# Performance work log

Measured on AMD Instinct MI355X. Metric: run time of the kernel, lower is better.

## Reference

```python
import jax, jax.numpy as jnp
import numpy as np

N = 100000   # total nodes
E = 1600000  # total edges
G = 1000     # graphs in batch
NPG = N // G # nodes per graph
IN = 128
HID = 128
LBL = 100
EMB = 32


def setup_inputs() -> dict:
    key = jax.random.key(0)
    ks = jax.random.split(key, 12)
    x = jax.random.normal(ks[0], (N, IN), dtype=jnp.float32)
    edge_index = jax.random.randint(ks[1], (2, E), 0, N, dtype=jnp.int32)
    drnl = jax.random.randint(ks[2], (N,), 0, LBL, dtype=jnp.int32)
    batch = (jnp.arange(N, dtype=jnp.int32) // NPG)
    target_local = jax.random.randint(ks[3], (2 * G,), 0, NPG, dtype=jnp.int32)
    ptr = jnp.arange(G + 1, dtype=jnp.int32) * NPG
    s = 0.02
    emb = s * jax.random.normal(ks[4], (LBL, EMB), dtype=jnp.float32)
    W1 = s * jax.random.normal(ks[5], (IN + EMB, HID), dtype=jnp.float32)
    b1 = jnp.zeros((HID,), jnp.float32)
    W2 = s * jax.random.normal(ks[6], (HID, HID), dtype=jnp.float32)
    b2 = jnp.zeros((HID,), jnp.float32)
    Wm1 = s * jax.random.normal(ks[7], (HID * 5, HID), dtype=jnp.float32)
    bm1 = jnp.zeros((HID,), jnp.float32)
    Wm2 = s * jax.random.normal(ks[8], (HID, 2), dtype=jnp.float32)
    bm2 = jnp.zeros((2,), jnp.float32)
    return {"x": x, "emb": emb, "W1": W1, "b1": b1, "W2": W2, "b2": b2,
            "Wm1": Wm1, "bm1": bm1, "Wm2": Wm2, "bm2": bm2,
            "edge_index": edge_index, "drnl": drnl, "batch": batch,
            "target_local": target_local, "ptr": ptr}


def gcn_conv(h, W, b, src, dst, n):
    # PyG GCNConv: linear, add self-loops, symmetric deg norm, scatter-add, bias
    hw = h @ W
    deg = jax.ops.segment_sum(jnp.ones(src.shape[0], hw.dtype), dst,
                              num_segments=n) + 1.0  # +1 for self loop
    dinv = jax.lax.rsqrt(deg)
    norm = dinv[src] * dinv[dst]          # [E]
    msg = hw[src] * norm[:, None]          # [E, hid] gather + scale
    agg = jax.ops.segment_sum(msg, dst, num_segments=n)
    agg = agg + hw * (dinv * dinv)[:, None]  # self-loop message
    return agg + b


def reference(x, emb, W1, b1, W2, b2, Wm1, bm1, Wm2, bm2,
              edge_index, drnl, batch, target_local, ptr):
    src, dst = edge_index[0], edge_index[1]
    n = x.shape[0]
    z = jnp.concatenate([x, emb[drnl]], axis=1)          # [N, in+32]
    z = jax.nn.relu(gcn_conv(z, W1, b1, src, dst, n))    # [N, hid]
    z = jax.nn.relu(gcn_conv(z, W2, b2, src, dst, n))    # [N, hid]
    g = ptr.shape[0] - 1
    h_pool = jax.ops.segment_max(z, batch, num_segments=g)  # global_max_pool
    uv = target_local.reshape(g, 2) + ptr[:-1, None]     # global node ids
    h_u = z[uv[:, 0]]
    h_v = z[uv[:, 1]]
    feats = jnp.concatenate([h_u, h_v, jnp.abs(h_u - h_v), h_u * h_v, h_pool],
                            axis=1)                      # [G, 5*hid]
    hidm = jax.nn.relu(feats @ Wm1 + bm1)
    logits = hidm @ Wm2 + bm2                            # [G, 2]
    return logits
```

## Files before the change

### kernel.cpp

```cpp
#include <hip/hip_runtime.h>
#include <hip/hip_bf16.h>
#include <math.h>

static inline size_t align_up(size_t x, size_t a) { return (x + a - 1) / a * a; }

typedef short bf16x8 __attribute__((ext_vector_type(8)));
typedef float f32x4 __attribute__((ext_vector_type(4)));
typedef unsigned short u16x8 __attribute__((ext_vector_type(8)));
typedef int i32x4 __attribute__((ext_vector_type(4)));


#define NBUCK 512
#define BCAP 8192

__global__ __launch_bounds__(256) void bin_kernel(
    const int* __restrict__ src, const int* __restrict__ dst,
    int* __restrict__ bcnt, long long* __restrict__ staging, int E) {
  __shared__ int lcnt[NBUCK];
  __shared__ int gbase[NBUCK];
  __shared__ int lidx[NBUCK];
  const int tid = threadIdx.x;
  const int base = blockIdx.x * 4096;
  lcnt[tid] = 0; lcnt[tid + 256] = 0;
  lidx[tid] = 0; lidx[tid + 256] = 0;
  __syncthreads();
#pragma unroll
  for (int j = 0; j < 4; ++j) {
    const int idx = base + j * 1024 + tid * 4;
    if (idx + 3 < E) {
      const i32x4 d4 = __builtin_nontemporal_load((const i32x4*)(dst + idx));
#pragma unroll
      for (int c = 0; c < 4; ++c) atomicAdd(&lcnt[d4[c] >> 8], 1);
    } else {
      for (int c = 0; c < 4; ++c)
        if (idx + c < E) atomicAdd(&lcnt[dst[idx + c] >> 8], 1);
    }
  }
  __syncthreads();
  {
    const int c0 = lcnt[tid];
    if (c0 > 0) gbase[tid] = atomicAdd(&bcnt[tid], c0);
    const int c1 = lcnt[tid + 256];
    if (c1 > 0) gbase[tid + 256] = atomicAdd(&bcnt[tid + 256], c1);
  }
  __syncthreads();
#pragma unroll
  for (int j = 0; j < 4; ++j) {
    const int idx = base + j * 1024 + tid * 4;
    if (idx + 3 < E) {
      const i32x4 d4 = __builtin_nontemporal_load((const i32x4*)(dst + idx));
      const i32x4 s4 = __builtin_nontemporal_load((const i32x4*)(src + idx));
#pragma unroll
      for (int c = 0; c < 4; ++c) {
        const int d = d4[c];
        const int bkt = d >> 8;
        const int i = atomicAdd(&lidx[bkt], 1);
        const int pos = gbase[bkt] + i;
        if (pos < BCAP)
          staging[(size_t)bkt * BCAP + pos] =
              (long long)(((unsigned long long)(unsigned)s4[c] << 32) | (unsigned)d);
      }
    } else {
      for (int c = 0; c < 4; ++c) {
        if (idx + c < E) {
          const int d = dst[idx + c];
          const int bkt = d >> 8;
          const int i = atomicAdd(&lidx[bkt], 1);
          const int pos = gbase[bkt] + i;
          if (pos < BCAP)
            staging[(size_t)bkt * BCAP + pos] =
                (long long)(((unsigned long long)(unsigned)src[idx + c] << 32) | (unsigned)d);
        }
      }
    }
  }
}

__global__ __launch_bounds__(512) void bscan_kernel(const int* __restrict__ bcnt,
                                                    int* __restrict__ bbase,
                                                    int* __restrict__ rowptr, int N, int E) {
  __shared__ int sm[NBUCK];
  const int t = threadIdx.x;
  const int v = bcnt[t];
  sm[t] = v;
  __syncthreads();
  for (int o = 1; o < NBUCK; o <<= 1) {
    int x = (t >= o) ? sm[t - o] : 0;
    __syncthreads();
    sm[t] += x;
    __syncthreads();
  }
  bbase[t] = sm[t] - v;
  if (t == 0) rowptr[N] = E;
}

__global__ __launch_bounds__(256) void csr_kernel(
    const long long* __restrict__ staging, const int* __restrict__ bcnt,
    const int* __restrict__ bbase, int* __restrict__ rowptr,
    float* __restrict__ dinv, int* __restrict__ esrc, int N) {
  __shared__ int c1[256];
  __shared__ int off[256];
  __shared__ int sm[256];
  const int b = blockIdx.x;
  const int tid = threadIdx.x;
  const int cnt = min(bcnt[b], BCAP);
  const int base = bbase[b];
  const long long* sp = staging + (size_t)b * BCAP;
  c1[tid] = 0;
  __syncthreads();
  for (int i = tid; i < cnt; i += 256) {
    const int d8 = ((int)sp[i]) & 255;
    atomicAdd(&c1[d8], 1);
  }
  __syncthreads();
  const int deg = c1[tid];
  sm[tid] = deg;
  __syncthreads();
  for (int o = 1; o < 256; o <<= 1) {
    int x = (tid >= o) ? sm[tid - o] : 0;
    __syncthreads();
    sm[tid] += x;
    __syncthreads();
  }
  off[tid] = sm[tid] - deg;
  const int node = b * 256 + tid;
  if (node < N) {
    rowptr[node] = base + off[tid];
    dinv[node] = rsqrtf((float)(deg + 1));
  }
  c1[tid] = 0;
  __syncthreads();
  for (int i = tid; i < cnt; i += 256) {
    const long long pr = sp[i];
    const int d8 = ((int)pr) & 255;
    const int idx = atomicAdd(&c1[d8], 1);
    esrc[base + off[d8] + idx] = (int)(unsigned)((unsigned long long)pr >> 32);
  }
}


__device__ __forceinline__ void bf16_split(float x, unsigned short& hi, unsigned short& lo) {
  unsigned u = __float_as_uint(x);
  unsigned r = (u + 0x7fffu + ((u >> 16) & 1u)) & 0xffff0000u;
  hi = (unsigned short)(r >> 16);
  float rem = x - __uint_as_float(r);
  unsigned u2 = __float_as_uint(rem);
  unsigned r2 = u2 + 0x7fffu + ((u2 >> 16) & 1u);
  lo = (unsigned short)(r2 >> 16);
}

__device__ __forceinline__ unsigned short bf16_rtn(float x) {
  unsigned u = __float_as_uint(x);
  return (unsigned short)((u + 0x7fffu + ((u >> 16) & 1u)) >> 16);
}

__global__ void wsplit_kernel(const float* __restrict__ W1, const float* __restrict__ W2,
                              unsigned short* __restrict__ w1hi, unsigned short* __restrict__ w1lo,
                              unsigned short* __restrict__ w2hi, unsigned short* __restrict__ w2lo) {
  int i = blockIdx.x * blockDim.x + threadIdx.x;
  const int t1 = 160 * 128;
  const int t2 = 128 * 128;
  const float* W;
  unsigned short *whi, *wlo;
  if (i < t1) {
    W = W1; whi = w1hi; wlo = w1lo;
  } else {
    i -= t1;
    if (i >= t2) return;
    W = W2; whi = w2hi; wlo = w2lo;
  }
  int k = i >> 7;
  int n = i & 127;
  unsigned short h, l;
  bf16_split(W[i], h, l);
  size_t idx = ((size_t)(((k >> 5) * 128 + n) * 4 + ((k >> 3) & 3)) << 3) + (k & 7);
  whi[idx] = h;
  wlo[idx] = l;
}


__global__ __launch_bounds__(512) void gemm_mfma_kernel(
    const float* __restrict__ A, const float* __restrict__ emb,
    const int* __restrict__ drnl,
    const unsigned short* __restrict__ whi, const unsigned short* __restrict__ wlo,
    unsigned short* __restrict__ outb, int n, int K) {
  __shared__ unsigned short smem[16896];
  const int tid = threadIdx.x;
  const int row0 = blockIdx.x * 128;
  const int w = tid >> 6;
  const int l = tid & 63;
  const int r = l & 15;
  const int q = l >> 4;
  const int grow = row0 + (w << 4) + r;
  const bool rowok = grow < n;
  const int nks = K >> 5;

  int embrow = 0;
  if (K > 128 && rowok) embrow = drnl[grow];

  f32x4 acc[8];
#pragma unroll
  for (int ct = 0; ct < 8; ++ct) {
    acc[ct][0] = 0.f; acc[ct][1] = 0.f; acc[ct][2] = 0.f; acc[ct][3] = 0.f;
  }

  u16x8 bst_h = *(const u16x8*)(whi + (size_t)tid * 8);
  u16x8 bst_l = *(const u16x8*)(wlo + (size_t)tid * 8);

  for (int ks = 0; ks < nks; ++ks) {
    const int k0 = (ks << 5) + (q << 3);
    float4 a0 = make_float4(0.f, 0.f, 0.f, 0.f), a1 = a0;
    if (rowok) {
      if (k0 < 128) {
        const float* ap = A + (size_t)grow * 128 + k0;
        a0 = *(const float4*)ap;
        a1 = *(const float4*)(ap + 4);
      } else {
        const float* ep = emb + (size_t)embrow * 32 + (k0 - 128);
        a0 = *(const float4*)ep;
        a1 = *(const float4*)(ep + 4);
      }
    }
    bf16x8 ah, al;
    {
      unsigned short h, lo_;
      bf16_split(a0.x, h, lo_); ah[0] = (short)h; al[0] = (short)lo_;
      bf16_split(a0.y, h, lo_); ah[1] = (short)h; al[1] = (short)lo_;
      bf16_split(a0.z, h, lo_); ah[2] = (short)h; al[2] = (short)lo_;
      bf16_split(a0.w, h, lo_); ah[3] = (short)h; al[3] = (short)lo_;
      bf16_split(a1.x, h, lo_); ah[4] = (short)h; al[4] = (short)lo_;
      bf16_split(a1.y, h, lo_); ah[5] = (short)h; al[5] = (short)lo_;
      bf16_split(a1.z, h, lo_); ah[6] = (short)h; al[6] = (short)lo_;
      bf16_split(a1.w, h, lo_); ah[7] = (short)h; al[7] = (short)lo_;
    }

    if (ks) __syncthreads();
    *(u16x8*)&smem[tid * 8] = bst_h;
    *(u16x8*)&smem[4096 + tid * 8] = bst_l;
    __syncthreads();

    if (ks + 1 < nks) {
      bst_h = *(const u16x8*)(whi + (size_t)(ks + 1) * 4096 + (size_t)tid * 8);
      bst_l = *(const u16x8*)(wlo + (size_t)(ks + 1) * 4096 + (size_t)tid * 8);
    }

#pragma unroll
    for (int ct = 0; ct < 8; ++ct) {
      const int boff = ((ct << 4) + r) * 32 + (q << 3);
      const bf16x8 bh = *(const bf16x8*)&smem[boff];
      const bf16x8 bl = *(const bf16x8*)&smem[4096 + boff];
      acc[ct] = __builtin_amdgcn_mfma_f32_16x16x32_bf16(ah, bh, acc[ct], 0, 0, 0);
      acc[ct] = __builtin_amdgcn_mfma_f32_16x16x32_bf16(al, bh, acc[ct], 0, 0, 0);
      acc[ct] = __builtin_amdgcn_mfma_f32_16x16x32_bf16(ah, bl, acc[ct], 0, 0, 0);
    }
  }

  __syncthreads();
#pragma unroll
  for (int ct = 0; ct < 8; ++ct) {
    const int col = (ct << 4) + r;
#pragma unroll
    for (int j = 0; j < 4; ++j) {
      const int row = (w << 4) + (q << 2) + j;
      smem[row * 132 + col] = bf16_rtn(acc[ct][j]);
    }
  }
  __syncthreads();
#pragma unroll
  for (int p = 0; p < 4; ++p) {
    const int idx = p * 512 + tid;
    const int row = idx >> 4;
    const int c8 = (idx & 15) * 8;
    const int gr = row0 + row;
    if (gr < n) {
      u16x8 v = *(const u16x8*)&smem[row * 132 + c8];
      *(u16x8*)(outb + (size_t)gr * 128 + c8) = v;
    }
  }
}


__global__ __launch_bounds__(512) void gemm_bf16a_kernel(
    const unsigned short* __restrict__ Ab,
    const unsigned short* __restrict__ whi, const unsigned short* __restrict__ wlo,
    unsigned short* __restrict__ outb, int n) {
  __shared__ unsigned short smem[16896];
  const int tid = threadIdx.x;
  const int row0 = blockIdx.x * 128;
  const int w = tid >> 6;
  const int l = tid & 63;
  const int r = l & 15;
  const int q = l >> 4;
  const int grow = row0 + (w << 4) + r;
  const bool rowok = grow < n;
  const int nks = 4;

  f32x4 acc[8];
#pragma unroll
  for (int ct = 0; ct < 8; ++ct) {
    acc[ct][0] = 0.f; acc[ct][1] = 0.f; acc[ct][2] = 0.f; acc[ct][3] = 0.f;
  }

  u16x8 bst_h = *(const u16x8*)(whi + (size_t)tid * 8);
  u16x8 bst_l = *(const u16x8*)(wlo + (size_t)tid * 8);

  for (int ks = 0; ks < nks; ++ks) {
    const int k0 = (ks << 5) + (q << 3);
    bf16x8 ah = {0,0,0,0,0,0,0,0};
    if (rowok) ah = *(const bf16x8*)(Ab + (size_t)grow * 128 + k0);

    if (ks) __syncthreads();
    *(u16x8*)&smem[tid * 8] = bst_h;
    *(u16x8*)&smem[4096 + tid * 8] = bst_l;
    __syncthreads();

    if (ks + 1 < nks) {
      bst_h = *(const u16x8*)(whi + (size_t)(ks + 1) * 4096 + (size_t)tid * 8);
      bst_l = *(const u16x8*)(wlo + (size_t)(ks + 1) * 4096 + (size_t)tid * 8);
    }

#pragma unroll
    for (int ct = 0; ct < 8; ++ct) {
      const int boff = ((ct << 4) + r) * 32 + (q << 3);
      const bf16x8 bh = *(const bf16x8*)&smem[boff];
      const bf16x8 bl = *(const bf16x8*)&smem[4096 + boff];
      acc[ct] = __builtin_amdgcn_mfma_f32_16x16x32_bf16(ah, bh, acc[ct], 0, 0, 0);
      acc[ct] = __builtin_amdgcn_mfma_f32_16x16x32_bf16(ah, bl, acc[ct], 0, 0, 0);
    }
  }

  __syncthreads();
#pragma unroll
  for (int ct = 0; ct < 8; ++ct) {
    const int col = (ct << 4) + r;
#pragma unroll
    for (int j = 0; j < 4; ++j) {
      const int row = (w << 4) + (q << 2) + j;
      smem[row * 132 + col] = bf16_rtn(acc[ct][j]);
    }
  }
  __syncthreads();
#pragma unroll
  for (int p = 0; p < 4; ++p) {
    const int idx = p * 512 + tid;
    const int row = idx >> 4;
    const int c8 = (idx & 15) * 8;
    const int gr = row0 + row;
    if (gr < n) {
      u16x8 v = *(const u16x8*)&smem[row * 132 + c8];
      *(u16x8*)(outb + (size_t)gr * 128 + c8) = v;
    }
  }
}


__global__ __launch_bounds__(256) void agg_kernel(
    const unsigned* __restrict__ hwb, const int* __restrict__ rowptr,
    const int* __restrict__ esrc, const float* __restrict__ dinv,
    const float* __restrict__ bias, float* __restrict__ zf,
    unsigned* __restrict__ zb, int n, int obf16) {
  const int widx = (blockIdx.x * blockDim.x + threadIdx.x) >> 6;
  if (widx >= n) return;
  const int wid = __builtin_amdgcn_readfirstlane(widx);
  const int lane = threadIdx.x & 63;
  const int start = rowptr[wid];
  const int end = rowptr[wid + 1];
  const float dn = dinv[wid];
  float ax = 0.f, ay = 0.f;
  int e = start;
  for (; e + 4 <= end; e += 4) {
    const int s0 = esrc[e + 0];
    const int s1 = esrc[e + 1];
    const int s2 = esrc[e + 2];
    const int s3 = esrc[e + 3];
    const float d0 = dinv[s0];
    const float d1 = dinv[s1];
    const float d2 = dinv[s2];
    const float d3 = dinv[s3];
    const unsigned u0 = hwb[(size_t)s0 * 64 + lane];
    const unsigned u1 = hwb[(size_t)s1 * 64 + lane];
    const unsigned u2 = hwb[(size_t)s2 * 64 + lane];
    const unsigned u3 = hwb[(size_t)s3 * 64 + lane];
    const float w0 = d0 * dn;
    const float w1 = d1 * dn;
    const float w2 = d2 * dn;
    const float w3 = d3 * dn;
    ax = fmaf(__uint_as_float(u0 << 16), w0, ax);
    ay = fmaf(__uint_as_float(u0 & 0xffff0000u), w0, ay);
    ax = fmaf(__uint_as_float(u1 << 16), w1, ax);
    ay = fmaf(__uint_as_float(u1 & 0xffff0000u), w1, ay);
    ax = fmaf(__uint_as_float(u2 << 16), w2, ax);
    ay = fmaf(__uint_as_float(u2 & 0xffff0000u), w2, ay);
    ax = fmaf(__uint_as_float(u3 << 16), w3, ax);
    ay = fmaf(__uint_as_float(u3 & 0xffff0000u), w3, ay);
  }
  for (; e < end; ++e) {
    const int s0 = esrc[e];
    const float w0 = dinv[s0] * dn;
    const unsigned u0 = hwb[(size_t)s0 * 64 + lane];
    ax = fmaf(__uint_as_float(u0 << 16), w0, ax);
    ay = fmaf(__uint_as_float(u0 & 0xffff0000u), w0, ay);
  }
  const float sw = dn * dn;
  const unsigned us = hwb[(size_t)wid * 64 + lane];
  ax = fmaf(__uint_as_float(us << 16), sw, ax);
  ay = fmaf(__uint_as_float(us & 0xffff0000u), sw, ay);
  const float2 bb = ((const float2*)bias)[lane];
  float ox = ax + bb.x, oy = ay + bb.y;
  ox = ox > 0.f ? ox : 0.f;
  oy = oy > 0.f ? oy : 0.f;
  if (obf16) {
    const unsigned pw = ((unsigned)bf16_rtn(oy) << 16) | (unsigned)bf16_rtn(ox);
    zb[(size_t)wid * 64 + lane] = pw;
  } else {
    float2 o; o.x = ox; o.y = oy;
    ((float2*)zf)[(size_t)wid * 64 + lane] = o;
  }
}


__global__ __launch_bounds__(128) void final_kernel(
    const float* __restrict__ z, const int* __restrict__ tloc,
    const int* __restrict__ ptr,
    const float* __restrict__ Wm1, const float* __restrict__ bm1,
    const float* __restrict__ Wm2, const float* __restrict__ bm2,
    float* __restrict__ out, int npg) {
  __shared__ float feats[640];
  __shared__ float hid[128];
  const int g = blockIdx.x;
  const int t = threadIdx.x;
  const float* zbk = z + (size_t)g * npg * 128;
  float m = -INFINITY;
  for (int r = 0; r < npg; ++r) m = fmaxf(m, zbk[(size_t)r * 128 + t]);
  feats[512 + t] = m;
  const int base = ptr[g];
  const int u = base + tloc[2 * g];
  const int v = base + tloc[2 * g + 1];
  const float hu = z[(size_t)u * 128 + t];
  const float hv = z[(size_t)v * 128 + t];
  feats[t] = hu;
  feats[128 + t] = hv;
  feats[256 + t] = fabsf(hu - hv);
  feats[384 + t] = hu * hv;
  __syncthreads();
  float acc = bm1[t];
#pragma unroll 8
  for (int k = 0; k < 640; ++k) acc = fmaf(feats[k], Wm1[(size_t)k * 128 + t], acc);
  hid[t] = acc > 0.f ? acc : 0.f;
  __syncthreads();
  if (t < 2) {
    float a = bm2[t];
    for (int j = 0; j < 128; ++j) a = fmaf(hid[j], Wm2[j * 2 + t], a);
    out[g * 2 + t] = a;
  }
}


extern "C" void kernel_launch(void* const* d_in, const int* in_sizes, int n_in,
                              void* d_out, int out_size, void* d_ws, size_t ws_size,
                              hipStream_t stream) {
  const float* x   = (const float*)d_in[0];
  const float* emb = (const float*)d_in[1];
  const float* W1  = (const float*)d_in[2];
  const float* b1  = (const float*)d_in[3];
  const float* W2  = (const float*)d_in[4];
  const float* b2  = (const float*)d_in[5];
  const float* Wm1 = (const float*)d_in[6];
  const float* bm1 = (const float*)d_in[7];
  const float* Wm2 = (const float*)d_in[8];
  const float* bm2 = (const float*)d_in[9];
  const int* eidx  = (const int*)d_in[10];
  const int* drnl  = (const int*)d_in[11];
  const int* tloc  = (const int*)d_in[13];
  const int* ptr   = (const int*)d_in[14];
  float* out = (float*)d_out;

  const int N = in_sizes[11];
  const int E = in_sizes[10] / 2;
  const int G = in_sizes[13] / 2;
  const int NPG = N / G;
  const int* srcp = eidx;
  const int* dstp = eidx + E;

  char* w = (char*)d_ws;
  size_t o = 0;
  auto alloc = [&](size_t bytes) {
    void* p = w + o;
    o = align_up(o + bytes, 256);
    return p;
  };
  int*   rowptr = (int*)alloc((size_t)(N + 1) * 4);
  float* dinv   = (float*)alloc((size_t)N * 4);
  int*   bcnt   = (int*)alloc(NBUCK * 4);
  int*   bbase  = (int*)alloc(NBUCK * 4);
  int*   esrc   = (int*)alloc((size_t)E * 4);
  unsigned short* hwb = (unsigned short*)alloc((size_t)N * 128 * 2);
  unsigned short* zb16 = (unsigned short*)alloc((size_t)N * 128 * 2);
  float* z      = (float*)alloc((size_t)N * 128 * 4);
  long long* staging = (long long*)z;
  unsigned short* w1hi = (unsigned short*)alloc((size_t)160 * 128 * 2);
  unsigned short* w1lo = (unsigned short*)alloc((size_t)160 * 128 * 2);
  unsigned short* w2hi = (unsigned short*)alloc((size_t)128 * 128 * 2);
  unsigned short* w2lo = (unsigned short*)alloc((size_t)128 * 128 * 2);

  const int nch = (E + 4095) / 4096;
  const int nbk = (N + 255) / 256;

  hipMemsetAsync(bcnt, 0, NBUCK * 4, stream);
  bin_kernel<<<nch, 256, 0, stream>>>(srcp, dstp, bcnt, staging, E);
  bscan_kernel<<<1, NBUCK, 0, stream>>>(bcnt, bbase, rowptr, N, E);
  csr_kernel<<<nbk, 256, 0, stream>>>(staging, bcnt, bbase, rowptr, dinv, esrc, N);

  wsplit_kernel<<<(160 * 128 + 128 * 128 + 255) / 256, 256, 0, stream>>>(
      W1, W2, w1hi, w1lo, w2hi, w2lo);

  gemm_mfma_kernel<<<(N + 127) / 128, 512, 0, stream>>>(x, emb, drnl, w1hi, w1lo, hwb, N, 160);
  agg_kernel<<<(N * 64 + 255) / 256, 256, 0, stream>>>((const unsigned*)hwb, rowptr, esrc,
                                                       dinv, b1, nullptr, (unsigned*)zb16, N, 1);
  gemm_bf16a_kernel<<<(N + 127) / 128, 512, 0, stream>>>(zb16, w2hi, w2lo, hwb, N);
  agg_kernel<<<(N * 64 + 255) / 256, 256, 0, stream>>>((const unsigned*)hwb, rowptr, esrc,
                                                       dinv, b2, z, nullptr, N, 0);
  final_kernel<<<G, 128, 0, stream>>>(z, tloc, ptr, Wm1, bm1, Wm2, bm2, out, NPG);
}
```

Measured before the change: 277.3 us.

## Pack staging to 32 bits, fuse bucket scan, store final z as bf16, unroll aggregation

Edge staging entries shrink from 64-bit pairs to 32-bit words (src<<8 | low dst byte), halving staging traffic in binning and CSR build. The separate bucket scan kernel is removed: each CSR block now redundantly scans the 512 bucket counts itself, saving one launch. The second aggregation writes bf16 instead of fp32, so the pooling/readout kernel reads half the bytes, at some precision cost. The aggregation loop is unrolled to 8 edges with all gathers issued first to raise memory-level parallelism. The packing assumes source ids fit in 24 bits.

Result: faster. 270.2 us (-2.6%).

```diff
diff --git a/kernel.cpp b/kernel.cpp
--- a/kernel.cpp
+++ b/kernel.cpp
@@ -15,7 +15,7 @@
 
 __global__ __launch_bounds__(256) void bin_kernel(
     const int* __restrict__ src, const int* __restrict__ dst,
-    int* __restrict__ bcnt, long long* __restrict__ staging, int E) {
+    int* __restrict__ bcnt, unsigned* __restrict__ staging, int E) {
   __shared__ int lcnt[NBUCK];
   __shared__ int gbase[NBUCK];
   __shared__ int lidx[NBUCK];
@@ -58,7 +58,7 @@
         const int pos = gbase[bkt] + i;
         if (pos < BCAP)
           staging[(size_t)bkt * BCAP + pos] =
-              (long long)(((unsigned long long)(unsigned)s4[c] << 32) | (unsigned)d);
+              ((unsigned)s4[c] << 8) | ((unsigned)d & 255u);
       }
     } else {
       for (int c = 0; c < 4; ++c) {
@@ -69,55 +69,50 @@
           const int pos = gbase[bkt] + i;
           if (pos < BCAP)
             staging[(size_t)bkt * BCAP + pos] =
-                (long long)(((unsigned long long)(unsigned)src[idx + c] << 32) | (unsigned)d);
+                ((unsigned)src[idx + c] << 8) | ((unsigned)d & 255u);
         }
       }
     }
   }
 }
 
-__global__ __launch_bounds__(512) void bscan_kernel(const int* __restrict__ bcnt,
-                                                    int* __restrict__ bbase,
-                                                    int* __restrict__ rowptr, int N, int E) {
-  __shared__ int sm[NBUCK];
-  const int t = threadIdx.x;
-  const int v = bcnt[t];
-  sm[t] = v;
-  __syncthreads();
-  for (int o = 1; o < NBUCK; o <<= 1) {
-    int x = (t >= o) ? sm[t - o] : 0;
-    __syncthreads();
-    sm[t] += x;
-    __syncthreads();
-  }
-  bbase[t] = sm[t] - v;
-  if (t == 0) rowptr[N] = E;
-}
 
 __global__ __launch_bounds__(256) void csr_kernel(
-    const long long* __restrict__ staging, const int* __restrict__ bcnt,
-    const int* __restrict__ bbase, int* __restrict__ rowptr,
-    float* __restrict__ dinv, int* __restrict__ esrc, int N) {
+    const unsigned* __restrict__ staging, const int* __restrict__ bcnt,
+    int* __restrict__ rowptr, float* __restrict__ dinv, int* __restrict__ esrc,
+    int N, int E) {
+  __shared__ int sb[NBUCK];
   __shared__ int c1[256];
   __shared__ int off[256];
   __shared__ int sm[256];
   const int b = blockIdx.x;
   const int tid = threadIdx.x;
+  sb[tid] = bcnt[tid];
+  sb[tid + 256] = bcnt[tid + 256];
+  __syncthreads();
+  for (int o = 1; o < NBUCK; o <<= 1) {
+    const int x0 = (tid >= o) ? sb[tid - o] : 0;
+    const int x1 = (tid + 256 >= o) ? sb[tid + 256 - o] : 0;
+    __syncthreads();
+    sb[tid] += x0;
+    sb[tid + 256] += x1;
+    __syncthreads();
+  }
   const int cnt = min(bcnt[b], BCAP);
-  const int base = bbase[b];
-  const long long* sp = staging + (size_t)b * BCAP;
+  const int base = sb[b] - bcnt[b];
+  if (b == 0 && tid == 0) rowptr[N] = E;
+  const unsigned* sp = staging + (size_t)b * BCAP;
   c1[tid] = 0;
   __syncthreads();
   for (int i = tid; i < cnt; i += 256) {
-    const int d8 = ((int)sp[i]) & 255;
-    atomicAdd(&c1[d8], 1);
+    atomicAdd(&c1[sp[i] & 255u], 1);
   }
   __syncthreads();
   const int deg = c1[tid];
   sm[tid] = deg;
   __syncthreads();
   for (int o = 1; o < 256; o <<= 1) {
-    int x = (tid >= o) ? sm[tid - o] : 0;
+    const int x = (tid >= o) ? sm[tid - o] : 0;
     __syncthreads();
     sm[tid] += x;
     __syncthreads();
@@ -131,10 +126,10 @@
   c1[tid] = 0;
   __syncthreads();
   for (int i = tid; i < cnt; i += 256) {
-    const long long pr = sp[i];
-    const int d8 = ((int)pr) & 255;
+    const unsigned pr = sp[i];
+    const int d8 = (int)(pr & 255u);
     const int idx = atomicAdd(&c1[d8], 1);
-    esrc[base + off[d8] + idx] = (int)(unsigned)((unsigned long long)pr >> 32);
+    esrc[base + off[d8] + idx] = (int)(pr >> 8);
   }
 }
 
@@ -152,6 +147,10 @@
 __device__ __forceinline__ unsigned short bf16_rtn(float x) {
   unsigned u = __float_as_uint(x);
   return (unsigned short)((u + 0x7fffu + ((u >> 16) & 1u)) >> 16);
+}
+
+__device__ __forceinline__ float bf16_to_f(unsigned short v) {
+  return __uint_as_float((unsigned)v << 16);
 }
 
 __global__ void wsplit_kernel(const float* __restrict__ W1, const float* __restrict__ W2,
@@ -357,8 +356,7 @@
 __global__ __launch_bounds__(256) void agg_kernel(
     const unsigned* __restrict__ hwb, const int* __restrict__ rowptr,
     const int* __restrict__ esrc, const float* __restrict__ dinv,
-    const float* __restrict__ bias, float* __restrict__ zf,
-    unsigned* __restrict__ zb, int n, int obf16) {
+    const float* __restrict__ bias, unsigned* __restrict__ zb, int n) {
   const int widx = (blockIdx.x * blockDim.x + threadIdx.x) >> 6;
   if (widx >= n) return;
   const int wid = __builtin_amdgcn_readfirstlane(widx);
@@ -368,31 +366,22 @@
   const float dn = dinv[wid];
   float ax = 0.f, ay = 0.f;
   int e = start;
-  for (; e + 4 <= end; e += 4) {
-    const int s0 = esrc[e + 0];
-    const int s1 = esrc[e + 1];
-    const int s2 = esrc[e + 2];
-    const int s3 = esrc[e + 3];
-    const float d0 = dinv[s0];
-    const float d1 = dinv[s1];
-    const float d2 = dinv[s2];
-    const float d3 = dinv[s3];
-    const unsigned u0 = hwb[(size_t)s0 * 64 + lane];
-    const unsigned u1 = hwb[(size_t)s1 * 64 + lane];
-    const unsigned u2 = hwb[(size_t)s2 * 64 + lane];
-    const unsigned u3 = hwb[(size_t)s3 * 64 + lane];
-    const float w0 = d0 * dn;
-    const float w1 = d1 * dn;
-    const float w2 = d2 * dn;
-    const float w3 = d3 * dn;
-    ax = fmaf(__uint_as_float(u0 << 16), w0, ax);
-    ay = fmaf(__uint_as_float(u0 & 0xffff0000u), w0, ay);
-    ax = fmaf(__uint_as_float(u1 << 16), w1, ax);
-    ay = fmaf(__uint_as_float(u1 & 0xffff0000u), w1, ay);
-    ax = fmaf(__uint_as_float(u2 << 16), w2, ax);
-    ay = fmaf(__uint_as_float(u2 & 0xffff0000u), w2, ay);
-    ax = fmaf(__uint_as_float(u3 << 16), w3, ax);
-    ay = fmaf(__uint_as_float(u3 & 0xffff0000u), w3, ay);
+  for (; e + 8 <= end; e += 8) {
+    int s[8];
+#pragma unroll
+    for (int k = 0; k < 8; ++k) s[k] = esrc[e + k];
+    unsigned u[8];
+#pragma unroll
+    for (int k = 0; k < 8; ++k) u[k] = hwb[(size_t)s[k] * 64 + lane];
+    float dv[8];
+#pragma unroll
+    for (int k = 0; k < 8; ++k) dv[k] = dinv[s[k]];
+#pragma unroll
+    for (int k = 0; k < 8; ++k) {
+      const float wk = dv[k] * dn;
+      ax = fmaf(__uint_as_float(u[k] << 16), wk, ax);
+      ay = fmaf(__uint_as_float(u[k] & 0xffff0000u), wk, ay);
+    }
   }
   for (; e < end; ++e) {
     const int s0 = esrc[e];
@@ -409,18 +398,13 @@
   float ox = ax + bb.x, oy = ay + bb.y;
   ox = ox > 0.f ? ox : 0.f;
   oy = oy > 0.f ? oy : 0.f;
-  if (obf16) {
-    const unsigned pw = ((unsigned)bf16_rtn(oy) << 16) | (unsigned)bf16_rtn(ox);
-    zb[(size_t)wid * 64 + lane] = pw;
-  } else {
-    float2 o; o.x = ox; o.y = oy;
-    ((float2*)zf)[(size_t)wid * 64 + lane] = o;
-  }
+  const unsigned pw = ((unsigned)bf16_rtn(oy) << 16) | (unsigned)bf16_rtn(ox);
+  zb[(size_t)wid * 64 + lane] = pw;
 }
 
 
 __global__ __launch_bounds__(128) void final_kernel(
-    const float* __restrict__ z, const int* __restrict__ tloc,
+    const unsigned short* __restrict__ zb, const int* __restrict__ tloc,
     const int* __restrict__ ptr,
     const float* __restrict__ Wm1, const float* __restrict__ bm1,
     const float* __restrict__ Wm2, const float* __restrict__ bm2,
@@ -429,15 +413,15 @@
   __shared__ float hid[128];
   const int g = blockIdx.x;
   const int t = threadIdx.x;
-  const float* zbk = z + (size_t)g * npg * 128;
+  const unsigned short* zbk = zb + (size_t)g * npg * 128;
   float m = -INFINITY;
-  for (int r = 0; r < npg; ++r) m = fmaxf(m, zbk[(size_t)r * 128 + t]);
+  for (int r = 0; r < npg; ++r) m = fmaxf(m, bf16_to_f(zbk[(size_t)r * 128 + t]));
   feats[512 + t] = m;
   const int base = ptr[g];
   const int u = base + tloc[2 * g];
   const int v = base + tloc[2 * g + 1];
-  const float hu = z[(size_t)u * 128 + t];
-  const float hv = z[(size_t)v * 128 + t];
+  const float hu = bf16_to_f(zb[(size_t)u * 128 + t]);
+  const float hv = bf16_to_f(zb[(size_t)v * 128 + t]);
   feats[t] = hu;
   feats[128 + t] = hv;
   feats[256 + t] = fabsf(hu - hv);
@@ -492,12 +476,11 @@
   int*   rowptr = (int*)alloc((size_t)(N + 1) * 4);
   float* dinv   = (float*)alloc((size_t)N * 4);
   int*   bcnt   = (int*)alloc(NBUCK * 4);
-  int*   bbase  = (int*)alloc(NBUCK * 4);
   int*   esrc   = (int*)alloc((size_t)E * 4);
-  unsigned short* hwb = (unsigned short*)alloc((size_t)N * 128 * 2);
-  unsigned short* zb16 = (unsigned short*)alloc((size_t)N * 128 * 2);
-  float* z      = (float*)alloc((size_t)N * 128 * 4);
-  long long* staging = (long long*)z;
+  unsigned short* hwb  = (unsigned short*)alloc((size_t)N * 128 * 2);
+  unsigned short* zb1  = (unsigned short*)alloc((size_t)N * 128 * 2);
+  unsigned short* zb2  = (unsigned short*)alloc((size_t)N * 128 * 2);
+  unsigned* staging = (unsigned*)zb2;
   unsigned short* w1hi = (unsigned short*)alloc((size_t)160 * 128 * 2);
   unsigned short* w1lo = (unsigned short*)alloc((size_t)160 * 128 * 2);
   unsigned short* w2hi = (unsigned short*)alloc((size_t)128 * 128 * 2);
@@ -508,17 +491,16 @@
 
   hipMemsetAsync(bcnt, 0, NBUCK * 4, stream);
   bin_kernel<<<nch, 256, 0, stream>>>(srcp, dstp, bcnt, staging, E);
-  bscan_kernel<<<1, NBUCK, 0, stream>>>(bcnt, bbase, rowptr, N, E);
-  csr_kernel<<<nbk, 256, 0, stream>>>(staging, bcnt, bbase, rowptr, dinv, esrc, N);
+  csr_kernel<<<nbk, 256, 0, stream>>>(staging, bcnt, rowptr, dinv, esrc, N, E);
 
   wsplit_kernel<<<(160 * 128 + 128 * 128 + 255) / 256, 256, 0, stream>>>(
       W1, W2, w1hi, w1lo, w2hi, w2lo);
 
   gemm_mfma_kernel<<<(N + 127) / 128, 512, 0, stream>>>(x, emb, drnl, w1hi, w1lo, hwb, N, 160);
   agg_kernel<<<(N * 64 + 255) / 256, 256, 0, stream>>>((const unsigned*)hwb, rowptr, esrc,
-                                                       dinv, b1, nullptr, (unsigned*)zb16, N, 1);
-  gemm_bf16a_kernel<<<(N + 127) / 128, 512, 0, stream>>>(zb16, w2hi, w2lo, hwb, N);
+                                                       dinv, b1, (unsigned*)zb1, N);
+  gemm_bf16a_kernel<<<(N + 127) / 128, 512, 0, stream>>>(zb1, w2hi, w2lo, hwb, N);
   agg_kernel<<<(N * 64 + 255) / 256, 256, 0, stream>>>((const unsigned*)hwb, rowptr, esrc,
-                                                       dinv, b2, z, nullptr, N, 0);
-  final_kernel<<<G, 128, 0, stream>>>(z, tloc, ptr, Wm1, bm1, Wm2, bm2, out, NPG);
-}
+                                                       dinv, b2, (unsigned*)zb2, N);
+  final_kernel<<<G, 128, 0, stream>>>(zb2, tloc, ptr, Wm1, bm1, Wm2, bm2, out, NPG);
+}
```
